# Kernel optimization log

Hardware: AMD Instinct MI355X
Metric: run time of the kernel (lower is better)

Reference implementation:

```python
import jax, jax.numpy as jnp
import numpy as np

SPATIAL_DECAY = 50.0
POS_SCALE = 1000.0  # spread positions so decay=50 gives realistic locality


def setup_inputs() -> dict:
    key = jax.random.key(0)
    k1, k2 = jax.random.split(key)
    N, D = 8192, 512
    features = jax.random.normal(k1, (N, D), dtype=jnp.float32)
    positions = jax.random.uniform(k2, (N, 2), dtype=jnp.float32) * POS_SCALE
    lambda_weight = jnp.asarray(0.5, dtype=jnp.float32)  # nn.Parameter init
    temperature = jnp.asarray(1.0, dtype=jnp.float32)    # nn.Parameter init
    return {"features": features, "positions": positions,
            "lambda_weight": lambda_weight, "temperature": temperature, "k": 20}


def reference(features, positions, lambda_weight, temperature, k):
    N = features.shape[0]
    # F.normalize(dim=1), eps=1e-12
    norms = jnp.linalg.norm(features, axis=1, keepdims=True)
    feat_norm = features / jnp.maximum(norms, 1e-12)
    sim = feat_norm @ feat_norm.T                                   # (N, N)
    # squared euclidean distances (cdist(p=2) then **2 == squared dist)
    sq = jnp.sum(positions * positions, axis=1)                      # (N,)
    d2 = jnp.maximum(sq[:, None] + sq[None, :] - 2.0 * (positions @ positions.T), 0.0)
    spatial = jnp.exp(-d2 / (2.0 * SPATIAL_DECAY ** 2))             # (N, N)
    lam = jax.nn.sigmoid(lambda_weight)
    adj = jax.nn.sigmoid((lam * sim + (1.0 - lam) * spatial) * temperature)
    # row-wise top-k mask, scatter 1.0 at top-k columns
    _, topk_idx = jax.lax.top_k(adj, k)                              # (N, k)
    rows = jnp.arange(N)[:, None]
    mask = jnp.zeros_like(adj).at[rows, topk_idx].set(1.0)
    return adj * mask, lam
```

## Files before the change

kernel.cpp:

```cpp
#include <hip/hip_runtime.h>
#include <hip/hip_fp16.h>
#include <math.h>

#define N 8192
#define D 512
#define KSEL 20
#define CAND_CAP 384
#define WINDOW 2.5e-3f
#define BS_EXTRA 6.2e-4f
#define ROWU 8192
#define FS_A 4096

typedef __attribute__((ext_vector_type(8))) short short8;
typedef __attribute__((ext_vector_type(4))) float f32x4;

__device__ __forceinline__ unsigned short f2bf(float x) {
  unsigned int u = __float_as_uint(x);
  unsigned int r = u + 0x7FFFu + ((u >> 16) & 1u);
  return (unsigned short)(r >> 16);
}

__device__ __forceinline__ unsigned int packh2(float a, float b) {
  return (unsigned int)__half_as_ushort(__float2half(a)) |
         ((unsigned int)__half_as_ushort(__float2half(b)) << 16);
}

__device__ __forceinline__ void gld16(const unsigned short* g, unsigned short* l) {
  __builtin_amdgcn_global_load_lds(
      (const __attribute__((address_space(1))) unsigned int*)g,
      (__attribute__((address_space(3))) unsigned int*)l, 16, 0, 0);
}

__device__ __forceinline__ int swz(int row, int cp) {
  return row * 64 + ((((cp >> 2) ^ (row & 15)) << 2) | (cp & 3));
}
__device__ __forceinline__ int swz4(int row, int q) {
  return row * 64 + ((q ^ (row & 15)) << 2);
}

__global__ __launch_bounds__(256) void prep_kernel(
    const float* __restrict__ feat, const float* __restrict__ pos,
    const float* __restrict__ lamw,
    float* __restrict__ normf, float* __restrict__ sqf,
    float* __restrict__ fn32, unsigned short* __restrict__ fnbf,
    float* __restrict__ out) {
  __shared__ float rowbuf[4][512];
  int w = threadIdx.x >> 6, lane = threadIdx.x & 63;
  float* rb = rowbuf[w];
  for (int i = 0; i < 8; i++) {
    int row = blockIdx.x * 32 + w * 8 + i;
    const float* f = feat + (size_t)row * D;
    float4 v0 = *(const float4*)(f + 4 * lane);
    float4 v1 = *(const float4*)(f + 256 + 4 * lane);
    *(float4*)&rb[4 * lane] = v0;
    *(float4*)&rb[256 + 4 * lane] = v1;
    __builtin_amdgcn_s_waitcnt(0);
    float s = 0.f;
    if (lane < 32) {
      int b = lane >> 3, j = lane & 7;
      const float* a = rb + b * 128 + j;
      float r = __fmul_rn(a[0], a[0]);
      #pragma unroll
      for (int k = 1; k < 16; k++)
        r = __fadd_rn(r, __fmul_rn(a[8 * k], a[8 * k]));
      r = __fadd_rn(r, __shfl_xor(r, 1, 64));
      r = __fadd_rn(r, __shfl_xor(r, 2, 64));
      r = __fadd_rn(r, __shfl_xor(r, 4, 64));
      r = __fadd_rn(r, __shfl_xor(r, 8, 64));
      r = __fadd_rn(r, __shfl_xor(r, 16, 64));
      s = r;
    }
    float st = __shfl(s, 0, 64);
    float nrm = fmaxf(__fsqrt_rn(st), 1e-12f);
    if (lane == 0) {
      normf[row] = nrm;
      float x = pos[2 * row], y = pos[2 * row + 1];
      sqf[row] = __fadd_rn(__fmul_rn(x, x), __fmul_rn(y, y));
      if (row == 0) {
        float e = (float)exp(-(double)lamw[0]);
        out[(size_t)N * N] = 1.0f / __fadd_rn(1.0f, e);
      }
    }
    float4 q0, q1;
    q0.x = v0.x / nrm; q0.y = v0.y / nrm; q0.z = v0.z / nrm; q0.w = v0.w / nrm;
    q1.x = v1.x / nrm; q1.y = v1.y / nrm; q1.z = v1.z / nrm; q1.w = v1.w / nrm;
    *(float4*)(fn32 + (size_t)row * D + 4 * lane) = q0;
    *(float4*)(fn32 + (size_t)row * D + 256 + 4 * lane) = q1;
    uint2 o0, o1;
    o0.x = (unsigned int)f2bf(q0.x) | ((unsigned int)f2bf(q0.y) << 16);
    o0.y = (unsigned int)f2bf(q0.z) | ((unsigned int)f2bf(q0.w) << 16);
    o1.x = (unsigned int)f2bf(q1.x) | ((unsigned int)f2bf(q1.y) << 16);
    o1.y = (unsigned int)f2bf(q1.z) | ((unsigned int)f2bf(q1.w) << 16);
    *(uint2*)(fnbf + (size_t)row * D + 4 * lane) = o0;
    *(uint2*)(fnbf + (size_t)row * D + 256 + 4 * lane) = o1;
  }
}

__global__ __launch_bounds__(256) void adj_kernel(
    const unsigned short* __restrict__ G,
    const float* __restrict__ pos, const float* __restrict__ sqf,
    const float* __restrict__ lamw, const float* __restrict__ temp,
    unsigned int* __restrict__ filt, int fs,
    unsigned int* __restrict__ out_u, int mode) {
  __shared__ __align__(16) unsigned char smem[32768];
  unsigned short* As = (unsigned short*)smem;
  unsigned short* Bs = As + 8192;
  unsigned int* tileT = (unsigned int*)smem;

  int L = blockIdx.x;
  int tid = threadIdx.x;

  if (L < 2048) {
    uint4 z = {0u, 0u, 0u, 0u};
    if (mode == 0) {
      size_t base = (size_t)L * 32768;
      #pragma unroll
      for (int it = 0; it < 32; it++)
        *(uint4*)(out_u + base + it * 1024 + tid * 4) = z;
    } else {
      #pragma unroll
      for (int it = 0; it < 16; it++) {
        int g = L * 16384 + it * 1024 + tid * 4;
        int r = g >> 12, c = g & 4095;
        *(uint4*)(out_u + (size_t)r * ROWU + 4096 + c) = z;
      }
    }
  }

  int by = (int)((129.0 - sqrt(129.0 * 129.0 - 8.0 * (double)L)) * 0.5);
  while (64 * (by + 1) - ((by + 1) * by) / 2 <= L) by++;
  while (64 * by - (by * (by - 1)) / 2 > L) by--;
  int bx = by + (L - (64 * by - (by * (by - 1)) / 2));

  int wave = tid >> 6, lane = tid & 63;
  int wr = (wave >> 1) * 64, wc = (wave & 1) * 64;
  int m = lane & 15, quad = lane >> 4;

  f32x4 acc[4][4];
  #pragma unroll
  for (int i = 0; i < 4; i++)
    #pragma unroll
    for (int j = 0; j < 4; j++) acc[i][j] = (f32x4){0.f, 0.f, 0.f, 0.f};

  for (int kt = 0; kt < D / 64; kt++) {
    #pragma unroll
    for (int i = 0; i < 4; i++) {
      int f = i * 256 + tid;
      int r = f >> 3, c = f & 7;
      int cs = (c + r) & 7;
      size_t goff = (size_t)r * D + kt * 64 + cs * 8;
      gld16(G + (size_t)(by * 128) * D + goff, &As[f * 8]);
      gld16(G + (size_t)(bx * 128) * D + goff, &Bs[f * 8]);
    }
    __syncthreads();
    #pragma unroll
    for (int h = 0; h < 2; h++) {
      short8 fa[4], fb[4];
      #pragma unroll
      for (int ti = 0; ti < 4; ti++) {
        int row = wr + ti * 16 + m;
        int cc = ((h * 4 + quad) - row) & 7;
        fa[ti] = *(const short8*)&As[row * 64 + cc * 8];
      }
      #pragma unroll
      for (int tj = 0; tj < 4; tj++) {
        int row = wc + tj * 16 + m;
        int cc = ((h * 4 + quad) - row) & 7;
        fb[tj] = *(const short8*)&Bs[row * 64 + cc * 8];
      }
      #pragma unroll
      for (int ti = 0; ti < 4; ti++)
        #pragma unroll
        for (int tj = 0; tj < 4; tj++)
          acc[ti][tj] = __builtin_amdgcn_mfma_f32_16x16x32_bf16(
              fa[ti], fb[tj], acc[ti][tj], 0, 0, 0);
    }
    __syncthreads();
  }

  float lam = 1.f / (1.f + __expf(-lamw[0]));
  float T = temp[0];
  float oml = 1.f - lam;
  bool offdiag = (bx != by);

  #pragma unroll
  for (int ti = 0; ti < 4; ti++) {
    int gi0 = by * 128 + wr + ti * 16 + quad * 4;
    float xi[4], yi[4], sqi[4];
    #pragma unroll
    for (int r = 0; r < 4; r++) {
      int gi = gi0 + r;
      xi[r] = pos[2 * gi]; yi[r] = pos[2 * gi + 1]; sqi[r] = sqf[gi];
    }
    #pragma unroll
    for (int tj = 0; tj < 4; tj++) {
      int gj = bx * 128 + wc + tj * 16 + m;
      float xj = pos[2 * gj], yj = pos[2 * gj + 1], sj = sqf[gj];
      f32x4 c = acc[ti][tj];
      float sv[4];
      #pragma unroll
      for (int r = 0; r < 4; r++) {
        float d2 = fmaxf(sqi[r] + sj - 2.f * (xi[r] * xj + yi[r] * yj), 0.f);
        float sp = __expf(-d2 * (1.f / 5000.f));
        sv[r] = (lam * c[r] + oml * sp) * T;
      }
      int cpL = (wc + tj * 16 + m) >> 1;
      #pragma unroll
      for (int r = 0; r < 4; r++) {
        float pv = __shfl_xor(sv[r], 1, 64);
        if (!(lane & 1)) {
          int rowL = wr + ti * 16 + quad * 4 + r;
          tileT[swz(rowL, cpL)] = packh2(sv[r], pv);
        }
      }
    }
  }
  __syncthreads();

  #pragma unroll
  for (int it = 0; it < 8; it++) {
    int idx4 = it * 256 + tid;
    int row = idx4 >> 4, q = idx4 & 15;
    uint4 v = *(uint4*)&tileT[swz4(row, q)];
    *(uint4*)(filt + (size_t)(by * 128 + row) * fs + bx * 64 + q * 4) = v;
  }

  if (offdiag) {
    #pragma unroll
    for (int it = 0; it < 8; it++) {
      int idx4 = it * 256 + tid;
      int c = idx4 >> 4, q = idx4 & 15;
      unsigned int wv[4];
      #pragma unroll
      for (int d = 0; d < 4; d++) {
        int p = q * 4 + d;
        unsigned int lo = tileT[swz(2 * p, c >> 1)];
        unsigned int hi = tileT[swz(2 * p + 1, c >> 1)];
        unsigned int h0 = (c & 1) ? (lo >> 16) : (lo & 0xFFFFu);
        unsigned int h1 = (c & 1) ? (hi >> 16) : (hi & 0xFFFFu);
        wv[d] = h0 | (h1 << 16);
      }
      uint4 v; v.x = wv[0]; v.y = wv[1]; v.z = wv[2]; v.w = wv[3];
      *(uint4*)(filt + (size_t)(bx * 128 + c) * fs + by * 64 + q * 4) = v;
    }
  }
}

__global__ __launch_bounds__(256, 6) void topk_kernel(
    const float* __restrict__ pos, const float* __restrict__ sqf,
    const float* __restrict__ lamw, const float* __restrict__ temp,
    const float* __restrict__ fn32,
    const unsigned int* __restrict__ filt, int fs,
    float* __restrict__ out, int doZero) {
  __shared__ float Tm[64 * 64];
  __shared__ float ai[D];
  __shared__ int   redi[2][4];
  __shared__ int   candIdx[CAND_CAP];
  __shared__ float candV[CAND_CAP];
  __shared__ int   selIdx[KSEL];
  __shared__ float selVal[KSEL];
  __shared__ int   cnt;

  int row = blockIdx.x, t = threadIdx.x;
  int lane = t & 63, wid = t >> 6;
  float* orow = out + (size_t)row * N;
  const uint4* fu4 = (const uint4*)(filt + (size_t)row * fs);
  const float* fn_i = fn32 + (size_t)row * D;

  float rv[32];
  #pragma unroll
  for (int q = 0; q < 4; q++) {
    uint4 u = fu4[t + 256 * q];
    unsigned int w[4] = {u.x, u.y, u.z, u.w};
    #pragma unroll
    for (int d = 0; d < 4; d++) {
      __half2 h2 = *reinterpret_cast<__half2*>(&w[d]);
      rv[8 * q + 2 * d]     = __low2float(h2);
      rv[8 * q + 2 * d + 1] = __high2float(h2);
    }
  }
  for (int k = t; k < D; k += 256) ai[k] = fn_i[k];
  if (t == 0) cnt = 0;
  __syncthreads();

  if (doZero) {
    float4 z4 = {0.f, 0.f, 0.f, 0.f};
    #pragma unroll
    for (int i = 0; i < 4; i++) *(float4*)&orow[4 * t + 1024 * i] = z4;
  }

  float lo = -1.0f, hi = 1.5f;
  for (int it = 0; it < 12; it++) {
    float mid = 0.5f * (lo + hi);
    int c = 0;
    #pragma unroll
    for (int q = 0; q < 32; q++) c += (rv[q] >= mid) ? 1 : 0;
    #pragma unroll
    for (int off = 32; off > 0; off >>= 1) c += __shfl_down(c, off, 64);
    if (lane == 0) redi[it & 1][wid] = c;
    __syncthreads();
    int tot = redi[it & 1][0] + redi[it & 1][1] + redi[it & 1][2] + redi[it & 1][3];
    if (tot >= KSEL) lo = mid; else hi = mid;
  }

  float thr = lo - (WINDOW + BS_EXTRA);
  #pragma unroll
  for (int q = 0; q < 32; q++) {
    if (rv[q] >= thr) {
      int p = atomicAdd(&cnt, 1);
      if (p < CAND_CAP) candIdx[p] = 8 * (t + 256 * (q >> 3)) + (q & 7);
    }
  }
  __syncthreads();
  int ncand = min(cnt, CAND_CAP);

  float lamf;
  { float e = (float)exp(-(double)lamw[0]); lamf = 1.0f / __fadd_rn(1.0f, e); }
  float omlf = __fadd_rn(1.0f, -lamf);
  float Tf = temp[0];
  float sq_i = sqf[row];
  float xi = pos[2 * row], yi = pos[2 * row + 1];
  int c4 = t >> 2, sub = t & 3;
  int slot = (c4 + 16 * sub) & 63;

  for (int g = 0; g < ncand; g += 64) {
    int sidx = g + c4;
    int sj = candIdx[(sidx < ncand) ? sidx : 0];
    const float* fj = fn32 + (size_t)sj * D + sub * 16;
    float accv = 0.0f;
    int myIdx = g + t;
    float4 pv[4];
    #pragma unroll
    for (int q = 0; q < 4; q++) pv[q] = *(const float4*)(fj + q * 4);
    for (int ck = 0; ck < 8; ck++) {
      __syncthreads();
      #pragma unroll
      for (int q = 0; q < 4; q++) {
        int kl = sub * 16 + q * 4;
        Tm[(kl + 0) * 64 + slot] = pv[q].x;
        Tm[(kl + 1) * 64 + slot] = pv[q].y;
        Tm[(kl + 2) * 64 + slot] = pv[q].z;
        Tm[(kl + 3) * 64 + slot] = pv[q].w;
      }
      __syncthreads();
      if (ck < 7) {
        #pragma unroll
        for (int q = 0; q < 4; q++) pv[q] = *(const float4*)(fj + (ck + 1) * 64 + q * 4);
      }
      if (t < 64) {
        int kk = ck * 64;
        for (int kl = 0; kl < 64; kl++) {
          int s = (t + 16 * (kl >> 4)) & 63;
          accv = __fmaf_rn(ai[kk + kl], Tm[kl * 64 + s], accv);
        }
      }
    }
    if (t < 64 && myIdx < ncand) {
      int j = candIdx[myIdx];
      float xj = pos[2 * j], yj = pos[2 * j + 1];
      float dot2 = __fmaf_rn(yi, yj, __fmul_rn(xi, xj));
      float Ssum = __fadd_rn(sq_i, sqf[j]);
      float d2 = fmaxf(__fadd_rn(Ssum, -__fmul_rn(2.0f, dot2)), 0.0f);
      float arg = (-d2) / 5000.0f;
      float sp = (float)exp((double)arg);
      float u = __fmul_rn(__fadd_rn(__fmul_rn(lamf, accv), __fmul_rn(omlf, sp)), Tf);
      float e = (float)exp(-(double)u);
      candV[myIdx] = 1.0f / __fadd_rn(1.0f, e);
    }
  }

  if (t < 64) {
    for (int s = 0; s < KSEL; s++) {
      float bu = -1.0f; int bj = N, bs = 0;
      for (int c = t; c < ncand; c += 64) {
        float v = candV[c]; int j = candIdx[c];
        if (v > bu || (v == bu && j < bj)) { bu = v; bj = j; bs = c; }
      }
      #pragma unroll
      for (int off = 32; off > 0; off >>= 1) {
        float ov = __shfl_down(bu, off, 64);
        int   oj = __shfl_down(bj, off, 64);
        int   os = __shfl_down(bs, off, 64);
        if (ov > bu || (ov == bu && oj < bj)) { bu = ov; bj = oj; bs = os; }
      }
      if (t == 0) { selIdx[s] = bj; selVal[s] = bu; candV[bs] = -1.0f; }
      __builtin_amdgcn_s_waitcnt(0);
    }
  }
  __syncthreads();
  if (t < KSEL) orow[selIdx[t]] = selVal[t];
}

extern "C" void kernel_launch(void* const* d_in, const int* in_sizes, int n_in,
                              void* d_out, int out_size, void* d_ws, size_t ws_size,
                              hipStream_t stream) {
  const float* feat = (const float*)d_in[0];
  const float* pos  = (const float*)d_in[1];
  const float* lamw = (const float*)d_in[2];
  const float* temp = (const float*)d_in[3];
  float* out = (float*)d_out;
  unsigned int* out_u = (unsigned int*)d_out;

  float* normf = (float*)d_ws;
  float* sqf   = normf + N;
  float* fn32  = sqf + N;
  unsigned short* fnbf = (unsigned short*)(fn32 + (size_t)N * D);
  unsigned int* filtA = (unsigned int*)(fnbf + (size_t)N * D);
  size_t needA = (size_t)2 * N * 4 + (size_t)N * D * 4 + (size_t)N * D * 2 +
                 (size_t)N * FS_A * 4;
  size_t needB = (size_t)2 * N * 4 + (size_t)N * D * 4 + (size_t)N * D * 2;

  prep_kernel<<<N / 32, 256, 0, stream>>>(feat, pos, lamw, normf, sqf,
                                          fn32, fnbf, out);
  if (ws_size >= needA) {
    adj_kernel<<<2080, 256, 0, stream>>>(fnbf, pos, sqf, lamw, temp,
                                         filtA, FS_A, out_u, 0);
    topk_kernel<<<N, 256, 0, stream>>>(pos, sqf, lamw, temp, fn32,
                                       filtA, FS_A, out, 0);
  } else {
    (void)needB;
    adj_kernel<<<2080, 256, 0, stream>>>(fnbf, pos, sqf, lamw, temp,
                                         out_u, ROWU, out_u, 1);
    topk_kernel<<<N, 256, 0, stream>>>(pos, sqf, lamw, temp, fn32,
                                       out_u, ROWU, out, 1);
  }
}
```

Measured before the change: 582.0 us.

## Give each candidate its own thread for fp32 rescoring dot products

The exact fp32 rescoring of top-k candidates no longer stages 64-candidate tiles through a shared-memory transpose. Each of up to 256 threads now computes one candidate's full 512-length dot product straight from global memory, with register double-buffering. This removes the per-chunk block barriers and the single active wave during the FMA loop. The candidate cap drops from 384 to 256 and the launch-bounds occupancy hint goes from 6 to 4, which risks overflow on rows with many near-threshold candidates and strided, uncoalesced global reads.

Result: no change. 570.8 us (-1.9%).

```diff
diff --git a/kernel.cpp b/kernel.cpp
--- a/kernel.cpp
+++ b/kernel.cpp
@@ -5,7 +5,7 @@
 #define N 8192
 #define D 512
 #define KSEL 20
-#define CAND_CAP 384
+#define CAND_CAP 256
 #define WINDOW 2.5e-3f
 #define BS_EXTRA 6.2e-4f
 #define ROWU 8192
@@ -246,13 +246,12 @@
   }
 }
 
-__global__ __launch_bounds__(256, 6) void topk_kernel(
+__global__ __launch_bounds__(256, 4) void topk_kernel(
     const float* __restrict__ pos, const float* __restrict__ sqf,
     const float* __restrict__ lamw, const float* __restrict__ temp,
     const float* __restrict__ fn32,
     const unsigned int* __restrict__ filt, int fs,
     float* __restrict__ out, int doZero) {
-  __shared__ float Tm[64 * 64];
   __shared__ float ai[D];
   __shared__ int   redi[2][4];
   __shared__ int   candIdx[CAND_CAP];
@@ -320,54 +319,42 @@
   float Tf = temp[0];
   float sq_i = sqf[row];
   float xi = pos[2 * row], yi = pos[2 * row + 1];
-  int c4 = t >> 2, sub = t & 3;
-  int slot = (c4 + 16 * sub) & 63;
-
-  for (int g = 0; g < ncand; g += 64) {
-    int sidx = g + c4;
-    int sj = candIdx[(sidx < ncand) ? sidx : 0];
-    const float* fj = fn32 + (size_t)sj * D + sub * 16;
+
+  if (t < ncand) {
+    int j = candIdx[t];
+    const float* fj = fn32 + (size_t)j * D;
     float accv = 0.0f;
-    int myIdx = g + t;
-    float4 pv[4];
-    #pragma unroll
-    for (int q = 0; q < 4; q++) pv[q] = *(const float4*)(fj + q * 4);
-    for (int ck = 0; ck < 8; ck++) {
-      __syncthreads();
+    float4 buf[4], nxt[4];
+    #pragma unroll
+    for (int q = 0; q < 4; q++) buf[q] = *(const float4*)(fj + q * 4);
+    for (int c16 = 0; c16 < 32; c16++) {
+      if (c16 < 31) {
+        #pragma unroll
+        for (int q = 0; q < 4; q++)
+          nxt[q] = *(const float4*)(fj + (c16 + 1) * 16 + q * 4);
+      }
       #pragma unroll
       for (int q = 0; q < 4; q++) {
-        int kl = sub * 16 + q * 4;
-        Tm[(kl + 0) * 64 + slot] = pv[q].x;
-        Tm[(kl + 1) * 64 + slot] = pv[q].y;
-        Tm[(kl + 2) * 64 + slot] = pv[q].z;
-        Tm[(kl + 3) * 64 + slot] = pv[q].w;
-      }
-      __syncthreads();
-      if (ck < 7) {
-        #pragma unroll
-        for (int q = 0; q < 4; q++) pv[q] = *(const float4*)(fj + (ck + 1) * 64 + q * 4);
-      }
-      if (t < 64) {
-        int kk = ck * 64;
-        for (int kl = 0; kl < 64; kl++) {
-          int s = (t + 16 * (kl >> 4)) & 63;
-          accv = __fmaf_rn(ai[kk + kl], Tm[kl * 64 + s], accv);
-        }
-      }
-    }
-    if (t < 64 && myIdx < ncand) {
-      int j = candIdx[myIdx];
-      float xj = pos[2 * j], yj = pos[2 * j + 1];
-      float dot2 = __fmaf_rn(yi, yj, __fmul_rn(xi, xj));
-      float Ssum = __fadd_rn(sq_i, sqf[j]);
-      float d2 = fmaxf(__fadd_rn(Ssum, -__fmul_rn(2.0f, dot2)), 0.0f);
-      float arg = (-d2) / 5000.0f;
-      float sp = (float)exp((double)arg);
-      float u = __fmul_rn(__fadd_rn(__fmul_rn(lamf, accv), __fmul_rn(omlf, sp)), Tf);
-      float e = (float)exp(-(double)u);
-      candV[myIdx] = 1.0f / __fadd_rn(1.0f, e);
-    }
-  }
+        float4 a4 = *(const float4*)&ai[c16 * 16 + q * 4];
+        accv = __fmaf_rn(a4.x, buf[q].x, accv);
+        accv = __fmaf_rn(a4.y, buf[q].y, accv);
+        accv = __fmaf_rn(a4.z, buf[q].z, accv);
+        accv = __fmaf_rn(a4.w, buf[q].w, accv);
+      }
+      #pragma unroll
+      for (int q = 0; q < 4; q++) buf[q] = nxt[q];
+    }
+    float xj = pos[2 * j], yj = pos[2 * j + 1];
+    float dot2 = __fmaf_rn(yi, yj, __fmul_rn(xi, xj));
+    float Ssum = __fadd_rn(sq_i, sqf[j]);
+    float d2 = fmaxf(__fadd_rn(Ssum, -__fmul_rn(2.0f, dot2)), 0.0f);
+    float arg = (-d2) / 5000.0f;
+    float sp = (float)exp((double)arg);
+    float u = __fmul_rn(__fadd_rn(__fmul_rn(lamf, accv), __fmul_rn(omlf, sp)), Tf);
+    float e = (float)exp(-(double)u);
+    candV[t] = 1.0f / __fadd_rn(1.0f, e);
+  }
+  __syncthreads();
 
   if (t < 64) {
     for (int s = 0; s < KSEL; s++) {
@@ -408,7 +395,6 @@
   unsigned int* filtA = (unsigned int*)(fnbf + (size_t)N * D);
   size_t needA = (size_t)2 * N * 4 + (size_t)N * D * 4 + (size_t)N * D * 2 +
                  (size_t)N * FS_A * 4;
-  size_t needB = (size_t)2 * N * 4 + (size_t)N * D * 4 + (size_t)N * D * 2;
 
   prep_kernel<<<N / 32, 256, 0, stream>>>(feat, pos, lamw, normf, sqf,
                                           fn32, fnbf, out);
@@ -418,7 +404,6 @@
     topk_kernel<<<N, 256, 0, stream>>>(pos, sqf, lamw, temp, fn32,
                                        filtA, FS_A, out, 0);
   } else {
-    (void)needB;
     adj_kernel<<<2080, 256, 0, stream>>>(fnbf, pos, sqf, lamw, temp,
                                          out_u, ROWU, out_u, 1);
     topk_kernel<<<N, 256, 0, stream>>>(pos, sqf, lamw, temp, fn32,
```
